# Optimization experiments

Hardware: AMD Instinct MI355X
Metric: run time of the kernel (lower is better)

## Reference

```python
import jax, jax.numpy as jnp
import numpy as np

CH = 64
GROUPS = 32
EPS = 1e-5


def setup_inputs() -> dict:
    key = jax.random.key(0)
    ks = jax.random.split(key, 10)
    b, c, h, w = 4, CH, 64, 64
    x = jax.random.normal(ks[0], (b, c, h, w), dtype=jnp.float32)
    s = 1.0 / np.sqrt(c)
    Wq = jax.random.normal(ks[1], (c, c), dtype=jnp.float32) * s
    bq = jnp.zeros((c,), dtype=jnp.float32)
    Wk = jax.random.normal(ks[2], (c, c), dtype=jnp.float32) * s
    bk = jnp.zeros((c,), dtype=jnp.float32)
    Wv = jax.random.normal(ks[3], (c, c), dtype=jnp.float32) * s
    bv = jnp.zeros((c,), dtype=jnp.float32)
    Wo = jax.random.normal(ks[4], (c, c), dtype=jnp.float32) * s
    bo = jnp.zeros((c,), dtype=jnp.float32)
    gamma = jnp.ones((c,), dtype=jnp.float32)
    beta = jnp.zeros((c,), dtype=jnp.float32)
    return {"x": x, "Wq": Wq, "bq": bq, "Wk": Wk, "bk": bk,
            "Wv": Wv, "bv": bv, "Wo": Wo, "bo": bo,
            "gamma": gamma, "beta": beta}


def group_norm(x, gamma, beta):
    b, c, h, w = x.shape
    xg = x.reshape(b, GROUPS, c // GROUPS, h, w)
    mean = jnp.mean(xg, axis=(2, 3, 4), keepdims=True)
    var = jnp.var(xg, axis=(2, 3, 4), keepdims=True)
    xn = ((xg - mean) * jax.lax.rsqrt(var + EPS)).reshape(b, c, h, w)
    return xn * gamma[None, :, None, None] + beta[None, :, None, None]


def conv1x1(x, W, bias):
    # 1x1 conv == channel matmul: x [b,c,h,w], W [out,in]
    return jnp.einsum('bchw,oc->bohw', x, W) + bias[None, :, None, None]


def reference(x, Wq, bq, Wk, bk, Wv, bv, Wo, bo, gamma, beta):
    b, c, h, w = x.shape
    n = h * w
    xn = group_norm(x, gamma, beta)
    q = conv1x1(xn, Wq, bq).reshape(b, c, n)  # [b,c,n]
    k = conv1x1(xn, Wk, bk).reshape(b, c, n)
    v = conv1x1(xn, Wv, bv).reshape(b, c, n)
    scale = 1.0 / jnp.sqrt(jnp.asarray(c, dtype=x.dtype))
    # scores: q^T k -> [b, n_q, n_k]
    attn = jax.nn.softmax(jnp.einsum('bci,bcj->bij', q, k) * scale, axis=-1)
    # out = v @ attn^T -> [b, c, n_q]
    out = jnp.einsum('bcj,bij->bci', v, attn).reshape(b, c, h, w)
    return x + conv1x1(out, Wo, bo)
```

## Files before the change

kernel.cpp:

```cpp
#include <hip/hip_runtime.h>
#include <hip/hip_bf16.h>

#define NPOS 4096
#define KS 72

typedef __attribute__((ext_vector_type(4))) float f32x4;
typedef __attribute__((ext_vector_type(8))) short bf16x8;
typedef __attribute__((ext_vector_type(2))) int i32x2;

__device__ __forceinline__ short f2bf(float f) {
  union { __hip_bfloat16 h; short s; } u;
  u.h = __float2bfloat16(f);
  return u.s;
}
__device__ __forceinline__ int pack_bf16(float lo, float hi) {
  unsigned a = (unsigned short)f2bf(lo);
  unsigned b = (unsigned short)f2bf(hi);
  return (int)(a | (b << 16));
}
__device__ __forceinline__ bf16x8 cvt8(const float* p) {
  f32x4 u = *(const f32x4*)p;
  f32x4 v = *(const f32x4*)(p + 4);
  bf16x8 r;
  r[0] = f2bf(u.x); r[1] = f2bf(u.y); r[2] = f2bf(u.z); r[3] = f2bf(u.w);
  r[4] = f2bf(v.x); r[5] = f2bf(v.y); r[6] = f2bf(v.z); r[7] = f2bf(v.w);
  return r;
}

__global__ __launch_bounds__(256) void stats_kernel(const float* __restrict__ x,
                                                    float* __restrict__ stats) {
  const int bg = blockIdx.x;
  const f32x4* base = (const f32x4*)(x + (size_t)bg * 8192);
  float s = 0.f, ss = 0.f;
  for (int i = threadIdx.x; i < 2048; i += 256) {
    f32x4 v = base[i];
    s  += v.x + v.y + v.z + v.w;
    ss += v.x * v.x + v.y * v.y + v.z * v.z + v.w * v.w;
  }
  for (int off = 32; off; off >>= 1) {
    s  += __shfl_down(s, off, 64);
    ss += __shfl_down(ss, off, 64);
  }
  __shared__ float red[8];
  const int wave = threadIdx.x >> 6, lane = threadIdx.x & 63;
  if (lane == 0) { red[wave] = s; red[4 + wave] = ss; }
  __syncthreads();
  if (threadIdx.x == 0) {
    float S  = red[0] + red[1] + red[2] + red[3];
    float SS = red[4] + red[5] + red[6] + red[7];
    float mean = S * (1.f / 8192.f);
    float var  = SS * (1.f / 8192.f) - mean * mean;
    stats[2 * bg]     = mean;
    stats[2 * bg + 1] = rsqrtf(var + 1e-5f);
  }
}

__global__ __launch_bounds__(256) void qkv_kernel(
    const float* __restrict__ x,
    const float* __restrict__ Wq, const float* __restrict__ bq,
    const float* __restrict__ Wk, const float* __restrict__ bk,
    const float* __restrict__ Wv, const float* __restrict__ bv,
    const float* __restrict__ gamma, const float* __restrict__ beta,
    const float* __restrict__ stats,
    short* __restrict__ qT, short* __restrict__ kT, short* __restrict__ vC) {
  __shared__ short xn_lds[32 * KS];
  __shared__ short out_lds[32 * 200];

  const int tid  = threadIdx.x;
  const int b    = blockIdx.x >> 7;
  const int pt   = blockIdx.x & 127;
  const int p0   = pt << 5;
  const int wave = tid >> 6;
  const int lane = tid & 63;
  const int quad = lane >> 4;
  const int l16  = lane & 15;

  bf16x8 a_lo[3], a_hi[3];
  float bias_r[3][4];
  {
    const float* Wsrc[3] = {Wq, Wk, Wv};
    const float* Bsrc[3] = {bq, bk, bv};
#pragma unroll
    for (int t = 0; t < 3; t++) {
      const float* wr = Wsrc[t] + (size_t)(wave * 16 + l16) * 64;
      a_lo[t] = cvt8(wr + quad * 8);
      a_hi[t] = cvt8(wr + 32 + quad * 8);
#pragma unroll
      for (int r = 0; r < 4; r++) bias_r[t][r] = Bsrc[t][wave * 16 + quad * 4 + r];
    }
  }

  {
    const int ch = tid >> 2, pg = tid & 3;
    float mean = stats[b * 64 + 2 * (ch >> 1)];
    float rstd = stats[b * 64 + 2 * (ch >> 1) + 1];
    float sc = rstd * gamma[ch];
    float sh = beta[ch] - mean * sc;
    const float* src = x + ((size_t)(b * 64 + ch)) * NPOS + p0 + pg * 8;
    f32x4 v0 = *(const f32x4*)src;
    f32x4 v1 = *(const f32x4*)(src + 4);
    short* d = xn_lds + ch;
    d[(pg * 8 + 0) * KS] = f2bf(fmaf(v0.x, sc, sh));
    d[(pg * 8 + 1) * KS] = f2bf(fmaf(v0.y, sc, sh));
    d[(pg * 8 + 2) * KS] = f2bf(fmaf(v0.z, sc, sh));
    d[(pg * 8 + 3) * KS] = f2bf(fmaf(v0.w, sc, sh));
    d[(pg * 8 + 4) * KS] = f2bf(fmaf(v1.x, sc, sh));
    d[(pg * 8 + 5) * KS] = f2bf(fmaf(v1.y, sc, sh));
    d[(pg * 8 + 6) * KS] = f2bf(fmaf(v1.z, sc, sh));
    d[(pg * 8 + 7) * KS] = f2bf(fmaf(v1.w, sc, sh));
  }
  __syncthreads();

  const f32x4 zero4 = {0.f, 0.f, 0.f, 0.f};
#pragma unroll
  for (int n = 0; n < 2; n++) {
    const short* xr = xn_lds + (n * 16 + l16) * KS;
    bf16x8 b_lo = *(const bf16x8*)(xr + quad * 8);
    bf16x8 b_hi = *(const bf16x8*)(xr + 32 + quad * 8);
#pragma unroll
    for (int t = 0; t < 3; t++) {
      f32x4 c = zero4;
      c = __builtin_amdgcn_mfma_f32_16x16x32_bf16(a_lo[t], b_lo, c, 0, 0, 0);
      c = __builtin_amdgcn_mfma_f32_16x16x32_bf16(a_hi[t], b_hi, c, 0, 0, 0);
      i32x2 val;
      val.x = pack_bf16(c[0] + bias_r[t][0], c[1] + bias_r[t][1]);
      val.y = pack_bf16(c[2] + bias_r[t][2], c[3] + bias_r[t][3]);
      *(i32x2*)(out_lds + (n * 16 + l16) * 200 + t * 64 + wave * 16 + quad * 4) = val;
    }
  }
  __syncthreads();

  {
    const int p = tid >> 3, c8 = (tid & 7) << 3;
    short* qd = qT + ((size_t)(b * NPOS + p0 + p)) * 64 + c8;
    *(bf16x8*)qd = *(const bf16x8*)(out_lds + p * 200 + c8);
    short* kd = kT + ((size_t)(b * NPOS + p0 + p)) * 64 + c8;
    *(bf16x8*)kd = *(const bf16x8*)(out_lds + p * 200 + 64 + c8);
  }
  {
    const int ch = tid >> 2, pg = tid & 3;
    bf16x8 v;
#pragma unroll
    for (int i = 0; i < 8; i++) v[i] = out_lds[(pg * 8 + i) * 200 + 128 + ch];
    *(bf16x8*)(vC + ((size_t)(b * 64 + ch)) * NPOS + p0 + pg * 8) = v;
  }
}

__global__ __launch_bounds__(256, 4) void flash_part_kernel(
    const short* __restrict__ qT, const short* __restrict__ kT,
    const short* __restrict__ vC, float* __restrict__ part,
    float* __restrict__ ml) {
  __shared__ short K_lds[64 * KS];
  __shared__ short V_lds[64 * KS];
  __shared__ short P_lds[4 * 16 * KS];

  const int blk   = blockIdx.x;
  const int qt    = blk & 63;
  const int chunk = (blk >> 6) & 3;
  const int b     = blk >> 8;
  const int q0    = qt << 6;
  const int jc    = chunk << 10;
  const int tid   = threadIdx.x;
  const int wave  = tid >> 6;
  const int lane  = tid & 63;
  const int quad  = lane >> 4;
  const int l16   = lane & 15;
  const float scale = 0.125f;

  const short* qbase = qT + ((size_t)(b * NPOS + q0 + wave * 16 + l16)) * 64;
  bf16x8 bq0 = *(const bf16x8*)(qbase + quad * 8);
  bf16x8 bq1 = *(const bf16x8*)(qbase + 32 + quad * 8);

  const f32x4 zero4 = {0.f, 0.f, 0.f, 0.f};
  f32x4 o_acc[4] = {zero4, zero4, zero4, zero4};
  float m_i = -1e30f, l_i = 0.f;

  for (int kt = 0; kt < 16; kt++) {
    const int j0 = jc + (kt << 6);
    __syncthreads();
    {
      const int r  = tid >> 2;
      const int cc = (tid & 3) << 4;
      const bf16x8* ksrc = (const bf16x8*)(kT + ((size_t)(b * NPOS + j0 + r)) * 64 + cc);
      bf16x8* kdst = (bf16x8*)(K_lds + r * KS + cc);
      kdst[0] = ksrc[0]; kdst[1] = ksrc[1];
      const bf16x8* vsrc = (const bf16x8*)(vC + ((size_t)(b * 64 + r)) * NPOS + j0 + cc);
      bf16x8* vdst = (bf16x8*)(V_lds + r * KS + cc);
      vdst[0] = vsrc[0]; vdst[1] = vsrc[1];
    }
    __syncthreads();

    f32x4 st[4];
#pragma unroll
    for (int t = 0; t < 4; t++) {
      const short* kr = K_lds + (t * 16 + l16) * KS;
      bf16x8 ka0 = *(const bf16x8*)(kr + quad * 8);
      bf16x8 ka1 = *(const bf16x8*)(kr + 32 + quad * 8);
      f32x4 acc = zero4;
      acc = __builtin_amdgcn_mfma_f32_16x16x32_bf16(ka0, bq0, acc, 0, 0, 0);
      acc = __builtin_amdgcn_mfma_f32_16x16x32_bf16(ka1, bq1, acc, 0, 0, 0);
      st[t] = acc;
    }

    float rmax = -1e30f;
#pragma unroll
    for (int t = 0; t < 4; t++)
#pragma unroll
      for (int r = 0; r < 4; r++) rmax = fmaxf(rmax, st[t][r]);
    rmax = fmaxf(rmax, __shfl_xor(rmax, 16, 64));
    rmax = fmaxf(rmax, __shfl_xor(rmax, 32, 64));
    float mn = fmaxf(m_i, rmax * scale);
    float alpha = __expf(m_i - mn);
    float rsum = 0.f;
#pragma unroll
    for (int t = 0; t < 4; t++)
#pragma unroll
      for (int r = 0; r < 4; r++) {
        float pv = __expf(st[t][r] * scale - mn);
        st[t][r] = pv;
        rsum += pv;
      }
    rsum += __shfl_xor(rsum, 16, 64);
    rsum += __shfl_xor(rsum, 32, 64);
    l_i = l_i * alpha + rsum;
    m_i = mn;
#pragma unroll
    for (int t = 0; t < 4; t++) o_acc[t] *= alpha;

    short* pw = P_lds + wave * 16 * KS;
#pragma unroll
    for (int t = 0; t < 4; t++) {
      i32x2 val;
      val.x = pack_bf16(st[t][0], st[t][1]);
      val.y = pack_bf16(st[t][2], st[t][3]);
      *(i32x2*)(pw + l16 * KS + t * 16 + quad * 4) = val;
    }
    const short* pr = pw + l16 * KS;
    bf16x8 pb0 = *(const bf16x8*)(pr + quad * 8);
    bf16x8 pb1 = *(const bf16x8*)(pr + 32 + quad * 8);

#pragma unroll
    for (int t = 0; t < 4; t++) {
      const short* vr = V_lds + (t * 16 + l16) * KS;
      bf16x8 va0 = *(const bf16x8*)(vr + quad * 8);
      bf16x8 va1 = *(const bf16x8*)(vr + 32 + quad * 8);
      o_acc[t] = __builtin_amdgcn_mfma_f32_16x16x32_bf16(va0, pb0, o_acc[t], 0, 0, 0);
      o_acc[t] = __builtin_amdgcn_mfma_f32_16x16x32_bf16(va1, pb1, o_acc[t], 0, 0, 0);
    }
  }

  const size_t pbase = ((size_t)((b * 4 + chunk) * 64 + qt)) * 4096;
  const int col = wave * 16 + l16;
#pragma unroll
  for (int t = 0; t < 4; t++)
#pragma unroll
    for (int r = 0; r < 4; r++)
      part[pbase + (size_t)(t * 16 + quad * 4 + r) * 64 + col] = o_acc[t][r];
  if (quad == 0) {
    const size_t mlbase = ((size_t)((b * 4 + chunk) * 64 + qt)) * 128;
    ml[mlbase + col]      = m_i;
    ml[mlbase + 64 + col] = l_i;
  }
}

__global__ __launch_bounds__(256) void co_kernel(
    const float* __restrict__ part, const float* __restrict__ ml,
    const float* __restrict__ Wo, const float* __restrict__ bo,
    const float* __restrict__ x, float* __restrict__ y) {
  __shared__ float sm[4][32], sl[4][32], coef[4][32];
  __shared__ short attn_lds[32 * KS];
  __shared__ float y_lds[64 * 36];

  const int tid   = threadIdx.x;
  const int b     = blockIdx.x >> 7;
  const int pt    = blockIdx.x & 127;
  const int qt    = pt >> 1;
  const int rhalf = (pt & 1) << 5;
  const int p0    = pt << 5;
  const int wave  = tid >> 6;
  const int lane  = tid & 63;
  const int quad  = lane >> 4;
  const int l16   = lane & 15;

  const float* wr = Wo + (size_t)(wave * 16 + l16) * 64;
  bf16x8 a_lo = cvt8(wr + quad * 8);
  bf16x8 a_hi = cvt8(wr + 32 + quad * 8);

  if (tid < 128) {
    const int c = tid >> 5, r = tid & 31;
    const size_t mlbase = ((size_t)((b * 4 + c) * 64 + qt)) * 128;
    sm[c][r] = ml[mlbase + rhalf + r];
    sl[c][r] = ml[mlbase + 64 + rhalf + r];
  }
  __syncthreads();
  if (tid < 32) {
    float m0 = sm[0][tid], m1 = sm[1][tid], m2 = sm[2][tid], m3 = sm[3][tid];
    float ms = fmaxf(fmaxf(m0, m1), fmaxf(m2, m3));
    float w0 = __expf(m0 - ms), w1 = __expf(m1 - ms);
    float w2 = __expf(m2 - ms), w3 = __expf(m3 - ms);
    float lt = w0 * sl[0][tid] + w1 * sl[1][tid] + w2 * sl[2][tid] + w3 * sl[3][tid];
    float inv = 1.f / lt;
    coef[0][tid] = w0 * inv; coef[1][tid] = w1 * inv;
    coef[2][tid] = w2 * inv; coef[3][tid] = w3 * inv;
  }
  __syncthreads();

  {
    const int ch = tid >> 2, g = tid & 3;
    float acc[8];
#pragma unroll
    for (int i = 0; i < 8; i++) acc[i] = 0.f;
#pragma unroll
    for (int c = 0; c < 4; c++) {
      const f32x4* src = (const f32x4*)(part +
          ((size_t)((b * 4 + c) * 64 + qt)) * 4096 + (size_t)ch * 64 + rhalf + g * 8);
      f32x4 v0 = src[0], v1 = src[1];
      const float* cf = &coef[c][g * 8];
      acc[0] = fmaf(cf[0], v0.x, acc[0]); acc[1] = fmaf(cf[1], v0.y, acc[1]);
      acc[2] = fmaf(cf[2], v0.z, acc[2]); acc[3] = fmaf(cf[3], v0.w, acc[3]);
      acc[4] = fmaf(cf[4], v1.x, acc[4]); acc[5] = fmaf(cf[5], v1.y, acc[5]);
      acc[6] = fmaf(cf[6], v1.z, acc[6]); acc[7] = fmaf(cf[7], v1.w, acc[7]);
    }
#pragma unroll
    for (int i = 0; i < 8; i++) attn_lds[(g * 8 + i) * KS + ch] = f2bf(acc[i]);
  }
  __syncthreads();

  const f32x4 zero4 = {0.f, 0.f, 0.f, 0.f};
#pragma unroll
  for (int n = 0; n < 2; n++) {
    const short* ar = attn_lds + (n * 16 + l16) * KS;
    bf16x8 b_lo = *(const bf16x8*)(ar + quad * 8);
    bf16x8 b_hi = *(const bf16x8*)(ar + 32 + quad * 8);
    f32x4 c = zero4;
    c = __builtin_amdgcn_mfma_f32_16x16x32_bf16(a_lo, b_lo, c, 0, 0, 0);
    c = __builtin_amdgcn_mfma_f32_16x16x32_bf16(a_hi, b_hi, c, 0, 0, 0);
#pragma unroll
    for (int r = 0; r < 4; r++)
      y_lds[(wave * 16 + quad * 4 + r) * 36 + n * 16 + l16] = c[r];
  }
  __syncthreads();

  {
    const int ch = tid >> 2, pg = tid & 3;
    const size_t off = ((size_t)(b * 64 + ch)) * NPOS + p0 + pg * 8;
    const float* xs = x + off;
    float* dst = y + off;
    float bb = bo[ch];
    const float* ys = y_lds + ch * 36 + pg * 8;
    f32x4 x0 = *(const f32x4*)xs, x1 = *(const f32x4*)(xs + 4);
    f32x4 y0 = *(const f32x4*)ys, y1 = *(const f32x4*)(ys + 4);
    f32x4 o0 = {x0.x + bb + y0.x, x0.y + bb + y0.y, x0.z + bb + y0.z, x0.w + bb + y0.w};
    f32x4 o1 = {x1.x + bb + y1.x, x1.y + bb + y1.y, x1.z + bb + y1.z, x1.w + bb + y1.w};
    *(f32x4*)dst = o0;
    *(f32x4*)(dst + 4) = o1;
  }
}

extern "C" void kernel_launch(void* const* d_in, const int* in_sizes, int n_in,
                              void* d_out, int out_size, void* d_ws, size_t ws_size,
                              hipStream_t stream) {
  const float* x     = (const float*)d_in[0];
  const float* Wq    = (const float*)d_in[1];
  const float* bq    = (const float*)d_in[2];
  const float* Wk    = (const float*)d_in[3];
  const float* bk    = (const float*)d_in[4];
  const float* Wv    = (const float*)d_in[5];
  const float* bv    = (const float*)d_in[6];
  const float* Wo    = (const float*)d_in[7];
  const float* bo    = (const float*)d_in[8];
  const float* gamma = (const float*)d_in[9];
  const float* beta  = (const float*)d_in[10];
  float* y = (float*)d_out;

  char* ws = (char*)d_ws;
  float* stats = (float*)ws;
  short* qT   = (short*)(ws + 1024);
  short* kT   = (short*)(ws + 1024 + (1u << 21));
  short* vC   = (short*)(ws + 1024 + (2u << 21));
  float* part = (float*)(ws + 1024 + (3u << 21));
  float* ml   = (float*)(ws + 1024 + (11u << 21));

  stats_kernel<<<dim3(128), dim3(256), 0, stream>>>(x, stats);
  qkv_kernel<<<dim3(512), dim3(256), 0, stream>>>(x, Wq, bq, Wk, bk, Wv, bv,
                                                  gamma, beta, stats, qT, kT, vC);
  flash_part_kernel<<<dim3(1024), dim3(256), 0, stream>>>(qT, kT, vC, part, ml);
  co_kernel<<<dim3(512), dim3(256), 0, stream>>>(part, ml, Wo, bo, x, y);
}
```

Measured before the change: 130.0 us.

## Widen flash query tile to 128, split keys 8 ways, store partials in fp16

Result: slower. 135.9 us (+4.5%).

```diff
diff --git a/kernel.cpp b/kernel.cpp
--- a/kernel.cpp
+++ b/kernel.cpp
@@ -3,10 +3,13 @@
 
 #define NPOS 4096
 #define KS 72
+#define VS 80
 
 typedef __attribute__((ext_vector_type(4))) float f32x4;
 typedef __attribute__((ext_vector_type(8))) short bf16x8;
 typedef __attribute__((ext_vector_type(2))) int i32x2;
+typedef _Float16 f16;
+typedef __attribute__((ext_vector_type(8))) f16 f16x8;
 
 __device__ __forceinline__ short f2bf(float f) {
   union { __hip_bfloat16 h; short s; } u;
@@ -148,18 +151,17 @@
 
 __global__ __launch_bounds__(256, 4) void flash_part_kernel(
     const short* __restrict__ qT, const short* __restrict__ kT,
-    const short* __restrict__ vC, float* __restrict__ part,
+    const short* __restrict__ vC, f16* __restrict__ part,
     float* __restrict__ ml) {
-  __shared__ short K_lds[64 * KS];
-  __shared__ short V_lds[64 * KS];
-  __shared__ short P_lds[4 * 16 * KS];
+  __shared__ short V_lds[64 * VS];
+  __shared__ short P_lds[4][32 * VS];
 
   const int blk   = blockIdx.x;
-  const int qt    = blk & 63;
-  const int chunk = (blk >> 6) & 3;
+  const int qt    = blk & 31;
+  const int chunk = (blk >> 5) & 7;
   const int b     = blk >> 8;
-  const int q0    = qt << 6;
-  const int jc    = chunk << 10;
+  const int q0    = qt << 7;
+  const int jc    = chunk << 9;
   const int tid   = threadIdx.x;
   const int wave  = tid >> 6;
   const int lane  = tid & 63;
@@ -167,141 +169,170 @@
   const int l16   = lane & 15;
   const float scale = 0.125f;
 
-  const short* qbase = qT + ((size_t)(b * NPOS + q0 + wave * 16 + l16)) * 64;
-  bf16x8 bq0 = *(const bf16x8*)(qbase + quad * 8);
-  bf16x8 bq1 = *(const bf16x8*)(qbase + 32 + quad * 8);
+  bf16x8 bqf[2][2];
+#pragma unroll
+  for (int n = 0; n < 2; n++) {
+    const short* qbase = qT + ((size_t)(b * NPOS + q0 + wave * 32 + n * 16 + l16)) * 64;
+    bqf[n][0] = *(const bf16x8*)(qbase + quad * 8);
+    bqf[n][1] = *(const bf16x8*)(qbase + 32 + quad * 8);
+  }
 
   const f32x4 zero4 = {0.f, 0.f, 0.f, 0.f};
-  f32x4 o_acc[4] = {zero4, zero4, zero4, zero4};
-  float m_i = -1e30f, l_i = 0.f;
-
-  for (int kt = 0; kt < 16; kt++) {
+  f32x4 o_acc[2][4];
+#pragma unroll
+  for (int n = 0; n < 2; n++)
+#pragma unroll
+    for (int t = 0; t < 4; t++) o_acc[n][t] = zero4;
+  float m_i[2] = {-1e30f, -1e30f}, l_i[2] = {0.f, 0.f};
+
+  const short* kTb = kT + (size_t)b * NPOS * 64;
+
+  for (int kt = 0; kt < 8; kt++) {
     const int j0 = jc + (kt << 6);
     __syncthreads();
     {
-      const int r  = tid >> 2;
-      const int cc = (tid & 3) << 4;
-      const bf16x8* ksrc = (const bf16x8*)(kT + ((size_t)(b * NPOS + j0 + r)) * 64 + cc);
-      bf16x8* kdst = (bf16x8*)(K_lds + r * KS + cc);
-      kdst[0] = ksrc[0]; kdst[1] = ksrc[1];
-      const bf16x8* vsrc = (const bf16x8*)(vC + ((size_t)(b * 64 + r)) * NPOS + j0 + cc);
-      bf16x8* vdst = (bf16x8*)(V_lds + r * KS + cc);
-      vdst[0] = vsrc[0]; vdst[1] = vsrc[1];
+      const int ch = tid >> 2, go = (tid & 3) << 4;
+      const bf16x8* vsrc = (const bf16x8*)(vC + ((size_t)(b * 64 + ch)) * NPOS + j0 + go);
+      bf16x8* vdst = (bf16x8*)(V_lds + ch * VS + go);
+      vdst[0] = vsrc[0];
+      vdst[1] = vsrc[1];
     }
     __syncthreads();
 
-    f32x4 st[4];
+    f32x4 st[2][4];
 #pragma unroll
     for (int t = 0; t < 4; t++) {
-      const short* kr = K_lds + (t * 16 + l16) * KS;
+      const short* kr = kTb + ((size_t)(j0 + t * 16 + l16)) * 64;
       bf16x8 ka0 = *(const bf16x8*)(kr + quad * 8);
       bf16x8 ka1 = *(const bf16x8*)(kr + 32 + quad * 8);
-      f32x4 acc = zero4;
-      acc = __builtin_amdgcn_mfma_f32_16x16x32_bf16(ka0, bq0, acc, 0, 0, 0);
-      acc = __builtin_amdgcn_mfma_f32_16x16x32_bf16(ka1, bq1, acc, 0, 0, 0);
-      st[t] = acc;
-    }
-
-    float rmax = -1e30f;
-#pragma unroll
-    for (int t = 0; t < 4; t++)
-#pragma unroll
-      for (int r = 0; r < 4; r++) rmax = fmaxf(rmax, st[t][r]);
-    rmax = fmaxf(rmax, __shfl_xor(rmax, 16, 64));
-    rmax = fmaxf(rmax, __shfl_xor(rmax, 32, 64));
-    float mn = fmaxf(m_i, rmax * scale);
-    float alpha = __expf(m_i - mn);
-    float rsum = 0.f;
-#pragma unroll
-    for (int t = 0; t < 4; t++)
-#pragma unroll
-      for (int r = 0; r < 4; r++) {
-        float pv = __expf(st[t][r] * scale - mn);
-        st[t][r] = pv;
-        rsum += pv;
+#pragma unroll
+      for (int n = 0; n < 2; n++) {
+        f32x4 acc = zero4;
+        acc = __builtin_amdgcn_mfma_f32_16x16x32_bf16(ka0, bqf[n][0], acc, 0, 0, 0);
+        acc = __builtin_amdgcn_mfma_f32_16x16x32_bf16(ka1, bqf[n][1], acc, 0, 0, 0);
+        st[n][t] = acc;
       }
-    rsum += __shfl_xor(rsum, 16, 64);
-    rsum += __shfl_xor(rsum, 32, 64);
-    l_i = l_i * alpha + rsum;
-    m_i = mn;
-#pragma unroll
-    for (int t = 0; t < 4; t++) o_acc[t] *= alpha;
-
-    short* pw = P_lds + wave * 16 * KS;
+    }
+
+#pragma unroll
+    for (int n = 0; n < 2; n++) {
+      float rmax = -1e30f;
+#pragma unroll
+      for (int t = 0; t < 4; t++)
+#pragma unroll
+        for (int r = 0; r < 4; r++) rmax = fmaxf(rmax, st[n][t][r]);
+      rmax = fmaxf(rmax, __shfl_xor(rmax, 16, 64));
+      rmax = fmaxf(rmax, __shfl_xor(rmax, 32, 64));
+      float mn = fmaxf(m_i[n], rmax * scale);
+      float alpha = __expf(m_i[n] - mn);
+      float rsum = 0.f;
+#pragma unroll
+      for (int t = 0; t < 4; t++)
+#pragma unroll
+        for (int r = 0; r < 4; r++) {
+          float pv = __expf(st[n][t][r] * scale - mn);
+          st[n][t][r] = pv;
+          rsum += pv;
+        }
+      rsum += __shfl_xor(rsum, 16, 64);
+      rsum += __shfl_xor(rsum, 32, 64);
+      l_i[n] = l_i[n] * alpha + rsum;
+      m_i[n] = mn;
+#pragma unroll
+      for (int t = 0; t < 4; t++) o_acc[n][t] *= alpha;
+    }
+
+    short* pw = (short*)P_lds[wave];
+#pragma unroll
+    for (int n = 0; n < 2; n++)
+#pragma unroll
+      for (int t = 0; t < 4; t++) {
+        i32x2 val;
+        val.x = pack_bf16(st[n][t][0], st[n][t][1]);
+        val.y = pack_bf16(st[n][t][2], st[n][t][3]);
+        *(i32x2*)(pw + (n * 16 + l16) * VS + t * 16 + quad * 4) = val;
+      }
+    bf16x8 pb[2][2];
+#pragma unroll
+    for (int n = 0; n < 2; n++) {
+      const short* pr = pw + (n * 16 + l16) * VS;
+      pb[n][0] = *(const bf16x8*)(pr + quad * 8);
+      pb[n][1] = *(const bf16x8*)(pr + 32 + quad * 8);
+    }
+
 #pragma unroll
     for (int t = 0; t < 4; t++) {
-      i32x2 val;
-      val.x = pack_bf16(st[t][0], st[t][1]);
-      val.y = pack_bf16(st[t][2], st[t][3]);
-      *(i32x2*)(pw + l16 * KS + t * 16 + quad * 4) = val;
-    }
-    const short* pr = pw + l16 * KS;
-    bf16x8 pb0 = *(const bf16x8*)(pr + quad * 8);
-    bf16x8 pb1 = *(const bf16x8*)(pr + 32 + quad * 8);
-
-#pragma unroll
-    for (int t = 0; t < 4; t++) {
-      const short* vr = V_lds + (t * 16 + l16) * KS;
+      const short* vr = V_lds + (t * 16 + l16) * VS;
       bf16x8 va0 = *(const bf16x8*)(vr + quad * 8);
       bf16x8 va1 = *(const bf16x8*)(vr + 32 + quad * 8);
-      o_acc[t] = __builtin_amdgcn_mfma_f32_16x16x32_bf16(va0, pb0, o_acc[t], 0, 0, 0);
-      o_acc[t] = __builtin_amdgcn_mfma_f32_16x16x32_bf16(va1, pb1, o_acc[t], 0, 0, 0);
-    }
-  }
-
-  const size_t pbase = ((size_t)((b * 4 + chunk) * 64 + qt)) * 4096;
-  const int col = wave * 16 + l16;
-#pragma unroll
-  for (int t = 0; t < 4; t++)
-#pragma unroll
-    for (int r = 0; r < 4; r++)
-      part[pbase + (size_t)(t * 16 + quad * 4 + r) * 64 + col] = o_acc[t][r];
-  if (quad == 0) {
-    const size_t mlbase = ((size_t)((b * 4 + chunk) * 64 + qt)) * 128;
-    ml[mlbase + col]      = m_i;
-    ml[mlbase + 64 + col] = l_i;
+#pragma unroll
+      for (int n = 0; n < 2; n++) {
+        o_acc[n][t] = __builtin_amdgcn_mfma_f32_16x16x32_bf16(va0, pb[n][0], o_acc[n][t], 0, 0, 0);
+        o_acc[n][t] = __builtin_amdgcn_mfma_f32_16x16x32_bf16(va1, pb[n][1], o_acc[n][t], 0, 0, 0);
+      }
+    }
+  }
+
+  const size_t pbase = ((size_t)((b * 8 + chunk) * 32 + qt)) * 8192;
+#pragma unroll
+  for (int n = 0; n < 2; n++) {
+    const int col = wave * 32 + n * 16 + l16;
+#pragma unroll
+    for (int t = 0; t < 4; t++)
+#pragma unroll
+      for (int r = 0; r < 4; r++)
+        part[pbase + (size_t)(t * 16 + quad * 4 + r) * 128 + col] = (f16)o_acc[n][t][r];
+    if (quad == 0) {
+      const size_t mlbase = ((size_t)((b * 8 + chunk) * 32 + qt)) * 256;
+      ml[mlbase + col]       = m_i[n];
+      ml[mlbase + 128 + col] = l_i[n];
+    }
   }
 }
 
 __global__ __launch_bounds__(256) void co_kernel(
-    const float* __restrict__ part, const float* __restrict__ ml,
+    const f16* __restrict__ part, const float* __restrict__ ml,
     const float* __restrict__ Wo, const float* __restrict__ bo,
     const float* __restrict__ x, float* __restrict__ y) {
-  __shared__ float sm[4][32], sl[4][32], coef[4][32];
-  __shared__ short attn_lds[32 * KS];
+  __shared__ float sm[8][32], sl[8][32], coef[8][32];
+  __shared__ short attn_lds[32 * VS];
   __shared__ float y_lds[64 * 36];
 
-  const int tid   = threadIdx.x;
-  const int b     = blockIdx.x >> 7;
-  const int pt    = blockIdx.x & 127;
-  const int qt    = pt >> 1;
-  const int rhalf = (pt & 1) << 5;
-  const int p0    = pt << 5;
-  const int wave  = tid >> 6;
-  const int lane  = tid & 63;
-  const int quad  = lane >> 4;
-  const int l16   = lane & 15;
+  const int tid  = threadIdx.x;
+  const int b    = blockIdx.x >> 7;
+  const int pt   = blockIdx.x & 127;
+  const int fqt  = pt >> 2;
+  const int sub  = (pt & 3) << 5;
+  const int p0   = pt << 5;
+  const int wave = tid >> 6;
+  const int lane = tid & 63;
+  const int quad = lane >> 4;
+  const int l16  = lane & 15;
 
   const float* wr = Wo + (size_t)(wave * 16 + l16) * 64;
   bf16x8 a_lo = cvt8(wr + quad * 8);
   bf16x8 a_hi = cvt8(wr + 32 + quad * 8);
 
-  if (tid < 128) {
+  {
     const int c = tid >> 5, r = tid & 31;
-    const size_t mlbase = ((size_t)((b * 4 + c) * 64 + qt)) * 128;
-    sm[c][r] = ml[mlbase + rhalf + r];
-    sl[c][r] = ml[mlbase + 64 + rhalf + r];
+    const size_t mlbase = ((size_t)((b * 8 + c) * 32 + fqt)) * 256;
+    sm[c][r] = ml[mlbase + sub + r];
+    sl[c][r] = ml[mlbase + 128 + sub + r];
   }
   __syncthreads();
   if (tid < 32) {
-    float m0 = sm[0][tid], m1 = sm[1][tid], m2 = sm[2][tid], m3 = sm[3][tid];
-    float ms = fmaxf(fmaxf(m0, m1), fmaxf(m2, m3));
-    float w0 = __expf(m0 - ms), w1 = __expf(m1 - ms);
-    float w2 = __expf(m2 - ms), w3 = __expf(m3 - ms);
-    float lt = w0 * sl[0][tid] + w1 * sl[1][tid] + w2 * sl[2][tid] + w3 * sl[3][tid];
+    float ms = -1e30f;
+#pragma unroll
+    for (int c = 0; c < 8; c++) ms = fmaxf(ms, sm[c][tid]);
+    float w[8], lt = 0.f;
+#pragma unroll
+    for (int c = 0; c < 8; c++) {
+      w[c] = __expf(sm[c][tid] - ms);
+      lt = fmaf(w[c], sl[c][tid], lt);
+    }
     float inv = 1.f / lt;
-    coef[0][tid] = w0 * inv; coef[1][tid] = w1 * inv;
-    coef[2][tid] = w2 * inv; coef[3][tid] = w3 * inv;
+#pragma unroll
+    for (int c = 0; c < 8; c++) coef[c][tid] = w[c] * inv;
   }
   __syncthreads();
 
@@ -311,25 +342,22 @@
 #pragma unroll
     for (int i = 0; i < 8; i++) acc[i] = 0.f;
 #pragma unroll
-    for (int c = 0; c < 4; c++) {
-      const f32x4* src = (const f32x4*)(part +
-          ((size_t)((b * 4 + c) * 64 + qt)) * 4096 + (size_t)ch * 64 + rhalf + g * 8);
-      f32x4 v0 = src[0], v1 = src[1];
+    for (int c = 0; c < 8; c++) {
+      const f16x8 v = *(const f16x8*)(part +
+          (((size_t)((b * 8 + c) * 32 + fqt)) * 64 + ch) * 128 + sub + g * 8);
       const float* cf = &coef[c][g * 8];
-      acc[0] = fmaf(cf[0], v0.x, acc[0]); acc[1] = fmaf(cf[1], v0.y, acc[1]);
-      acc[2] = fmaf(cf[2], v0.z, acc[2]); acc[3] = fmaf(cf[3], v0.w, acc[3]);
-      acc[4] = fmaf(cf[4], v1.x, acc[4]); acc[5] = fmaf(cf[5], v1.y, acc[5]);
-      acc[6] = fmaf(cf[6], v1.z, acc[6]); acc[7] = fmaf(cf[7], v1.w, acc[7]);
-    }
-#pragma unroll
-    for (int i = 0; i < 8; i++) attn_lds[(g * 8 + i) * KS + ch] = f2bf(acc[i]);
+#pragma unroll
+      for (int i = 0; i < 8; i++) acc[i] = fmaf(cf[i], (float)v[i], acc[i]);
+    }
+#pragma unroll
+    for (int i = 0; i < 8; i++) attn_lds[(g * 8 + i) * VS + ch] = f2bf(acc[i]);
   }
   __syncthreads();
 
   const f32x4 zero4 = {0.f, 0.f, 0.f, 0.f};
 #pragma unroll
   for (int n = 0; n < 2; n++) {
-    const short* ar = attn_lds + (n * 16 + l16) * KS;
+    const short* ar = attn_lds + (n * 16 + l16) * VS;
     bf16x8 b_lo = *(const bf16x8*)(ar + quad * 8);
     bf16x8 b_hi = *(const bf16x8*)(ar + 32 + quad * 8);
     f32x4 c = zero4;
@@ -378,7 +406,7 @@
   short* qT   = (short*)(ws + 1024);
   short* kT   = (short*)(ws + 1024 + (1u << 21));
   short* vC   = (short*)(ws + 1024 + (2u << 21));
-  float* part = (float*)(ws + 1024 + (3u << 21));
+  f16*   part = (f16*)(ws + 1024 + (3u << 21));
   float* ml   = (float*)(ws + 1024 + (11u << 21));
 
   stats_kernel<<<dim3(128), dim3(256), 0, stream>>>(x, stats);
```
